# Kernel tuning notes

Hardware: AMD Instinct MI355X
Metric: run time of the kernel (lower is better)

## Reference

```python
import jax, jax.numpy as jnp
import numpy as np

D_HEAD = 64      # per-head dim (init d_head)
WINDOW = 64      # sliding_window_size
ROPE_BASE = 10000.0


def _rope(x):
    # x: [B, H, L, d] ; standard half-split rotary embedding over positions 0..L-1
    L, d = x.shape[-2], x.shape[-1]
    half = d // 2
    inv_freq = 1.0 / (ROPE_BASE ** (jnp.arange(half, dtype=jnp.float32) / half))
    ang = jnp.arange(L, dtype=jnp.float32)[:, None] * inv_freq  # [L, half]
    cos, sin = jnp.cos(ang), jnp.sin(ang)
    x1, x2 = x[..., :half], x[..., half:]
    return jnp.concatenate([x1 * cos - x2 * sin, x1 * sin + x2 * cos], axis=-1)


def setup_inputs() -> dict:
    key = jax.random.key(0)
    ks = jax.random.split(key, 4)
    B, L, D, H = 4, 2048, 2048, 2048
    nh = H // D_HEAD
    S = 16  # num_sinks
    u = jax.random.normal(ks[0], (B, L, D), jnp.float32)
    Wqkv = jax.random.normal(ks[1], (3 * H, D), jnp.float32) / np.sqrt(D)
    bqkv = jnp.zeros((3 * H,), jnp.float32)
    Wo = jax.random.normal(ks[2], (D, H), jnp.float32) / np.sqrt(H)
    bo = jnp.zeros((D,), jnp.float32)
    sinks = jax.random.normal(ks[3], (nh, S, D_HEAD), jnp.float32) / np.sqrt(D_HEAD)
    return {"u": u, "Wqkv": Wqkv, "bqkv": bqkv, "Wo": Wo, "bo": bo, "sinks": sinks}


def reference(u, Wqkv, bqkv, Wo, bo, sinks):
    B, L, D = u.shape
    d, w = D_HEAD, WINDOW
    nh, S, _ = sinks.shape
    scale = 1.0 / np.sqrt(d)

    qkv = u @ Wqkv.T + bqkv                         # [B, L, 3H]
    q, k, v = jnp.split(qkv, 3, axis=-1)
    heads = lambda x: x.reshape(B, L, nh, d).transpose(0, 2, 1, 3)  # [B, nh, L, d]
    q, k, v = heads(q), heads(k), heads(v)
    q, k = _rope(q), _rope(k)

    # Banded (sliding-window) attention in blocks of size w: query block i
    # attends key blocks {i-1, i, i+1} plus S global sink tokens.
    # Sink queries (prepended in the original) are discarded by O[:, :, -L:],
    # so we only compute attention for the L real queries.
    nb = L // w
    Qb = q.reshape(B, nh, nb, w, d)
    Kb = k.reshape(B, nh, nb, w, d)
    Vb = v.reshape(B, nh, nb, w, d)

    blk = jnp.arange(nb)[:, None] + jnp.arange(-1, 2)[None, :]   # [nb, 3]
    valid = (blk >= 0) & (blk < nb)
    blkc = jnp.clip(blk, 0, nb - 1)
    Kband = Kb[:, :, blkc].reshape(B, nh, nb, 3 * w, d)
    Vband = Vb[:, :, blkc].reshape(B, nh, nb, 3 * w, d)

    qpos = (jnp.arange(nb) * w)[:, None] + jnp.arange(w)          # [nb, w]
    kpos = ((blkc * w)[..., None] + jnp.arange(w)).reshape(nb, 3 * w)
    vmask = jnp.broadcast_to(valid[:, :, None], (nb, 3, w)).reshape(nb, 3 * w)
    mask = vmask[:, None, :] & (jnp.abs(qpos[:, :, None] - kpos[:, None, :]) <= w)  # [nb, w, 3w]

    s_band = jnp.einsum('bhnqd,bhnkd->bhnqk', Qb, Kband) * scale
    s_band = jnp.where(mask, s_band, -jnp.inf)
    s_sink = jnp.einsum('bhnqd,hsd->bhnqs', Qb, sinks) * scale    # sink K = sink param (no RoPE)
    p = jax.nn.softmax(jnp.concatenate([s_sink, s_band], axis=-1), axis=-1)

    O = (jnp.einsum('bhnqs,hsd->bhnqd', p[..., :S], sinks)        # sink V = sink param
         + jnp.einsum('bhnqk,bhnkd->bhnqd', p[..., S:], Vband))
    y = O.reshape(B, nh, L, d).transpose(0, 2, 1, 3).reshape(B, L, nh * d)
    return y @ Wo.T + bo
```

## Files before the change

kernel.cpp:

```cpp
#include <hip/hip_runtime.h>
#include <hip/hip_bf16.h>

typedef unsigned short u16;
typedef __attribute__((ext_vector_type(8))) short bf16x8;
typedef __attribute__((ext_vector_type(4))) float f32x4;

__device__ __forceinline__ u16 f2b(float f) {
  union { __hip_bfloat16 h; u16 u; } cv;
  cv.h = __float2bfloat16(f);
  return cv.u;
}
__device__ __forceinline__ float b2f(u16 u) {
  union { unsigned int i; float f; } cv;
  cv.i = ((unsigned int)u) << 16;
  return cv.f;
}

__global__ void cvt_bf16(const float* __restrict__ in, u16* __restrict__ out) {
  size_t i = ((size_t)blockIdx.x * 256 + threadIdx.x) * 4;
  float4 v = *(const float4*)(in + i);
  ushort4 o;
  o.x = f2b(v.x); o.y = f2b(v.y); o.z = f2b(v.z); o.w = f2b(v.w);
  *(ushort4*)(out + i) = o;
}

__global__ void rope_tab_k(float2* __restrict__ tab) {
  int t = blockIdx.x * 256 + threadIdx.x;
  int l = t >> 5, i = t & 31;
  float inv = powf(10000.0f, -(float)i * (1.0f / 32.0f));
  float ang = (float)l * inv;
  tab[t] = make_float2(cosf(ang), sinf(ang));
}

template<int NCOLS, bool ROPE>
__global__ __launch_bounds__(512, 2) void gemm_p(const u16* __restrict__ A,
                                                 const u16* __restrict__ Bm,
                                                 const float* __restrict__ bias,
                                                 u16* __restrict__ Cb,
                                                 float* __restrict__ Cf,
                                                 const float2* __restrict__ tab) {
  extern __shared__ char smem[];
  u16* Asl = (u16*)smem;
  u16* Bsl = (u16*)(smem + 65536);
  const int tid = threadIdx.x, lane = tid & 63, w = tid >> 6;
  const int wr = w >> 2, wcn = w & 3;
  const int fr = lane & 15, fk = lane >> 4;
  const int m0 = blockIdx.y * 256, n0 = blockIdx.x * 256;
  const int srow = lane >> 2;
  const int gslot = (lane & 3) ^ ((lane >> 3) & 3);
  const int c0 = w * 2, c1 = c0 + 1;
  const int sel = (fr >> 1) & 3;
  const int ka = (fk ^ sel) << 4;
  f32x4 acc[8][4] = {};

  auto stage = [&](int jj) {
    int slot = jj & 3;
    int kk = jj * 32 + gslot * 8;
    u16* Ad = Asl + slot * 8192;
    u16* Bd = Bsl + slot * 8192;
    const u16* gA0 = A  + (size_t)(m0 + c0 * 16 + srow) * 2048 + kk;
    const u16* gA1 = A  + (size_t)(m0 + c1 * 16 + srow) * 2048 + kk;
    const u16* gB0 = Bm + (size_t)(n0 + c0 * 16 + srow) * 2048 + kk;
    const u16* gB1 = Bm + (size_t)(n0 + c1 * 16 + srow) * 2048 + kk;
    __builtin_amdgcn_global_load_lds((const __attribute__((address_space(1))) unsigned int*)gA0,
        (__attribute__((address_space(3))) unsigned int*)(Ad + c0 * 512), 16, 0, 0);
    __builtin_amdgcn_global_load_lds((const __attribute__((address_space(1))) unsigned int*)gA1,
        (__attribute__((address_space(3))) unsigned int*)(Ad + c1 * 512), 16, 0, 0);
    __builtin_amdgcn_global_load_lds((const __attribute__((address_space(1))) unsigned int*)gB0,
        (__attribute__((address_space(3))) unsigned int*)(Bd + c0 * 512), 16, 0, 0);
    __builtin_amdgcn_global_load_lds((const __attribute__((address_space(1))) unsigned int*)gB1,
        (__attribute__((address_space(3))) unsigned int*)(Bd + c1 * 512), 16, 0, 0);
  };

  stage(0); stage(1); stage(2);
  asm volatile("s_waitcnt vmcnt(8)" ::: "memory");
  asm volatile("s_barrier" ::: "memory");

  for (int j = 0; j < 64; ++j) {
    if (j < 61) stage(j + 3);
    const char* Ab = (const char*)(Asl + (j & 3) * 8192);
    const char* Bb = (const char*)(Bsl + (j & 3) * 8192);
    bf16x8 af[8], bv[4];
    #pragma unroll
    for (int n = 0; n < 4; ++n)
      bv[n] = *(const bf16x8*)(Bb + (wcn * 64 + n * 16 + fr) * 64 + ka);
    #pragma unroll
    for (int m = 0; m < 8; ++m)
      af[m] = *(const bf16x8*)(Ab + (wr * 128 + m * 16 + fr) * 64 + ka);
    asm volatile("s_barrier" ::: "memory");
    asm volatile("s_waitcnt lgkmcnt(0)" ::: "memory");
    __builtin_amdgcn_sched_barrier(0);
    __builtin_amdgcn_s_setprio(1);
    #pragma unroll
    for (int m = 0; m < 8; ++m)
      #pragma unroll
      for (int n = 0; n < 4; ++n)
        acc[m][n] = __builtin_amdgcn_mfma_f32_16x16x32_bf16(af[m], bv[n], acc[m][n], 0, 0, 0);
    __builtin_amdgcn_s_setprio(0);
    __builtin_amdgcn_sched_barrier(0);
    if (j < 61)       asm volatile("s_waitcnt vmcnt(8)" ::: "memory");
    else if (j == 61) asm volatile("s_waitcnt vmcnt(4)" ::: "memory");
    else if (j == 62) asm volatile("s_waitcnt vmcnt(0)" ::: "memory");
    asm volatile("s_barrier" ::: "memory");
  }

  #pragma unroll
  for (int m = 0; m < 8; ++m) {
    int grow0 = m0 + wr * 128 + m * 16 + fk * 4;
    #pragma unroll
    for (int n = 0; n < 4; ++n) {
      int gcol = n0 + wcn * 64 + n * 16 + fr;
      if (ROPE) {
        if (gcol < 4096) {
          int c = gcol & 63;
          int i = c & 31;
          bool lo = c < 32;
          float bx = bias[gcol], bp = bias[gcol ^ 32];
          #pragma unroll
          for (int r = 0; r < 4; ++r) {
            int t = grow0 + r;
            float2 cs = tab[((t & 2047) << 5) + i];
            float xb = acc[m][n][r] + bx;
            float pb = acc[m][n ^ 2][r] + bp;
            float o = lo ? (xb * cs.x - pb * cs.y) : (pb * cs.y + xb * cs.x);
            Cb[(size_t)t * NCOLS + gcol] = f2b(o);
          }
        } else {
          float bx = bias[gcol];
          #pragma unroll
          for (int r = 0; r < 4; ++r)
            Cb[(size_t)(grow0 + r) * NCOLS + gcol] = f2b(acc[m][n][r] + bx);
        }
      } else {
        float bx = bias[gcol];
        #pragma unroll
        for (int r = 0; r < 4; ++r)
          Cf[(size_t)(grow0 + r) * NCOLS + gcol] = acc[m][n][r] + bx;
      }
    }
  }
}

#define PSTR 232
__global__ __launch_bounds__(256) void attn_k(const u16* __restrict__ qkv,
                                              const float* __restrict__ sinks,
                                              u16* __restrict__ O) {
  extern __shared__ char smem[];
  char* Kraw = smem;
  char* Qraw = smem + 28672;
  u16* Ps = (u16*)smem;
  u16* Vt = (u16*)(smem + 29696);
  char* tmpb = smem + 62464;
  const int tid = threadIdx.x, lane = tid & 63, wid = tid >> 6;
  const int fr = lane & 15, fk = lane >> 4;
  const int bx = blockIdx.x;
  const int n = bx & 31, h = (bx >> 5) & 31, b = bx >> 10;
  const size_t qrow0 = (size_t)b * 2048 + n * 64;

  for (int c = tid; c < 512; c += 256) {
    int row = c >> 3, colb = (c & 7) * 16;
    uint4 v = *(const uint4*)((const char*)(qkv + (qrow0 + row) * 6144 + h * 64) + colb);
    *(uint4*)(Qraw + ((row * 128 + colb) ^ ((row & 7) << 4))) = v;
  }
  {
    int row = tid >> 4, col4 = (tid & 15) * 4;
    float4 v = *(const float4*)(sinks + ((size_t)h * 16 + row) * 64 + col4);
    ushort4 o; o.x = f2b(v.x); o.y = f2b(v.y); o.z = f2b(v.z); o.w = f2b(v.w);
    *(ushort4*)(Kraw + ((row * 128 + col4 * 2) ^ ((row & 7) << 4))) = o;
  }
  for (int c = tid; c < 1536; c += 256) {
    int kidx = c >> 3, colb = (c & 7) * 16;
    int blk = n - 1 + (kidx >> 6);
    int blkc = min(max(blk, 0), 31);
    int kpos = blkc * 64 + (kidx & 63);
    uint4 v = *(const uint4*)((const char*)(qkv + ((size_t)b * 2048 + kpos) * 6144 + 2048 + h * 64) + colb);
    int row = 16 + kidx;
    *(uint4*)(Kraw + ((row * 128 + colb) ^ ((row & 7) << 4))) = v;
  }
  if (tid < 128) {
    int row = 208 + (tid >> 3), colb = (tid & 7) * 16;
    uint4 z = {0, 0, 0, 0};
    *(uint4*)(Kraw + ((row * 128 + colb) ^ ((row & 7) << 4))) = z;
  }
  __syncthreads();

  bf16x8 qf[2];
  {
    int qrow = wid * 16 + fr;
    #pragma unroll
    for (int kc = 0; kc < 2; ++kc)
      qf[kc] = *(const bf16x8*)(Qraw + ((qrow * 128 + kc * 64 + fk * 16) ^ ((qrow & 7) << 4)));
  }
  f32x4 sacc[14];
  #pragma unroll
  for (int g = 0; g < 14; ++g) {
    int key = g * 16 + fr;
    bf16x8 kf0 = *(const bf16x8*)(Kraw + ((key * 128 + fk * 16) ^ ((key & 7) << 4)));
    bf16x8 kf1 = *(const bf16x8*)(Kraw + ((key * 128 + 64 + fk * 16) ^ ((key & 7) << 4)));
    f32x4 a = {};
    a = __builtin_amdgcn_mfma_f32_16x16x32_bf16(qf[0], kf0, a, 0, 0, 0);
    a = __builtin_amdgcn_mfma_f32_16x16x32_bf16(qf[1], kf1, a, 0, 0, 0);
    sacc[g] = a;
  }
  float rowmax[4] = {-3e38f, -3e38f, -3e38f, -3e38f};
  #pragma unroll
  for (int g = 0; g < 14; ++g) {
    int key = g * 16 + fr;
    #pragma unroll
    for (int r = 0; r < 4; ++r) {
      float s = sacc[g][r] * 0.125f;
      bool valid;
      if (key < 16) valid = true;
      else if (key < 208) {
        int kidx = key - 16;
        int blk = n - 1 + (kidx >> 6);
        int kpos = blk * 64 + (kidx & 63);
        int qpos = n * 64 + wid * 16 + fk * 4 + r;
        valid = (blk >= 0) && (blk < 32) && (qpos - kpos <= 64) && (kpos - qpos <= 64);
      } else valid = false;
      s = valid ? s : -1e30f;
      sacc[g][r] = s;
      rowmax[r] = fmaxf(rowmax[r], s);
    }
  }
  #pragma unroll
  for (int d = 1; d < 16; d <<= 1)
    #pragma unroll
    for (int r = 0; r < 4; ++r)
      rowmax[r] = fmaxf(rowmax[r], __shfl_xor(rowmax[r], d));
  float rowsum[4] = {0, 0, 0, 0};
  #pragma unroll
  for (int g = 0; g < 14; ++g)
    #pragma unroll
    for (int r = 0; r < 4; ++r) {
      float p = __expf(sacc[g][r] - rowmax[r]);
      sacc[g][r] = p;
      rowsum[r] += p;
    }
  #pragma unroll
  for (int d = 1; d < 16; d <<= 1)
    #pragma unroll
    for (int r = 0; r < 4; ++r)
      rowsum[r] += __shfl_xor(rowsum[r], d);
  __syncthreads();

  #pragma unroll
  for (int g = 0; g < 14; ++g)
    #pragma unroll
    for (int r = 0; r < 4; ++r)
      Ps[(wid * 16 + fk * 4 + r) * PSTR + g * 16 + fr] = f2b(sacc[g][r]);

  {
    u16* tw = (u16*)(tmpb + wid * 1088);
    const int g = lane >> 3, s = lane & 7;
    if (wid < 2) {
      int key = wid * 8 + g;
      float4 v0 = *(const float4*)(sinks + ((size_t)h * 16 + key) * 64 + s * 8);
      float4 v1 = *(const float4*)(sinks + ((size_t)h * 16 + key) * 64 + s * 8 + 4);
      u16* dst = tw + g * 68 + s * 8;
      dst[0] = f2b(v0.x); dst[1] = f2b(v0.y); dst[2] = f2b(v0.z); dst[3] = f2b(v0.w);
      dst[4] = f2b(v1.x); dst[5] = f2b(v1.y); dst[6] = f2b(v1.z); dst[7] = f2b(v1.w);
      u16 col[8];
      #pragma unroll
      for (int k = 0; k < 8; ++k) col[k] = tw[k * 68 + lane];
      *(bf16x8*)(Vt + lane * 256 + ((wid ^ (lane & 7)) * 8)) = *(bf16x8*)col;
    } else {
      bf16x8 z = {};
      *(bf16x8*)(Vt + lane * 256 + (((24 + wid) ^ (lane & 7)) * 8)) = z;
    }
    for (int it = 0; it < 6; ++it) {
      int kidx = it * 32 + wid * 8 + g;
      int blk = n - 1 + (kidx >> 6);
      int blkc = min(max(blk, 0), 31);
      int kpos = blkc * 64 + (kidx & 63);
      uint4 v = *(const uint4*)(qkv + ((size_t)b * 2048 + kpos) * 6144 + 4096 + h * 64 + s * 8);
      *(uint4*)(tw + g * 68 + s * 8) = v;
      u16 col[8];
      #pragma unroll
      for (int k = 0; k < 8; ++k) col[k] = tw[k * 68 + lane];
      int gi = 2 + it * 4 + wid;
      *(bf16x8*)(Vt + lane * 256 + ((gi ^ (lane & 7)) * 8)) = *(bf16x8*)col;
    }
  }
  __syncthreads();

  f32x4 oacc[4] = {};
  #pragma unroll
  for (int kc = 0; kc < 7; ++kc) {
    bf16x8 pf = *(const bf16x8*)(Ps + (wid * 16 + fr) * PSTR + kc * 32 + fk * 8);
    #pragma unroll
    for (int gd = 0; gd < 4; ++gd) {
      bf16x8 vf = *(const bf16x8*)(Vt + (gd * 16 + fr) * 256 + (((kc * 4 + fk) ^ (fr & 7)) * 8));
      oacc[gd] = __builtin_amdgcn_mfma_f32_16x16x32_bf16(pf, vf, oacc[gd], 0, 0, 0);
    }
  }
  #pragma unroll
  for (int gd = 0; gd < 4; ++gd)
    #pragma unroll
    for (int r = 0; r < 4; ++r) {
      int qrl = wid * 16 + fk * 4 + r;
      float v = oacc[gd][r] / rowsum[r];
      O[(qrow0 + qrl) * 2048 + h * 64 + gd * 16 + fr] = f2b(v);
    }
}

extern "C" void kernel_launch(void* const* d_in, const int* in_sizes, int n_in,
                              void* d_out, int out_size, void* d_ws, size_t ws_size,
                              hipStream_t stream) {
  const float* u     = (const float*)d_in[0];
  const float* Wqkv  = (const float*)d_in[1];
  const float* bqkv  = (const float*)d_in[2];
  const float* Wo    = (const float*)d_in[3];
  const float* bo    = (const float*)d_in[4];
  const float* sinks = (const float*)d_in[5];
  float* out = (float*)d_out;

  char* ws = (char*)d_ws;
  u16* u_bf   = (u16*)ws;
  u16* w1_bf  = (u16*)(ws + 33554432);
  u16* qkv_bf = (u16*)(ws + 58720256);
  float2* tab = (float2*)(ws + 159383552);
  u16* O_bf  = u_bf;
  u16* w2_bf = w1_bf;

  hipFuncSetAttribute((const void*)gemm_p<6144, true>,
                      hipFuncAttributeMaxDynamicSharedMemorySize, 131072);
  hipFuncSetAttribute((const void*)gemm_p<2048, false>,
                      hipFuncAttributeMaxDynamicSharedMemorySize, 131072);
  hipFuncSetAttribute((const void*)attn_k,
                      hipFuncAttributeMaxDynamicSharedMemorySize, 66816);

  cvt_bf16<<<16384, 256, 0, stream>>>(u, u_bf);
  cvt_bf16<<<12288, 256, 0, stream>>>(Wqkv, w1_bf);
  rope_tab_k<<<256, 256, 0, stream>>>(tab);
  gemm_p<6144, true><<<dim3(24, 32), 512, 131072, stream>>>(u_bf, w1_bf, bqkv, qkv_bf, nullptr, tab);
  attn_k<<<4096, 256, 66816, stream>>>(qkv_bf, sinks, O_bf);
  cvt_bf16<<<4096, 256, 0, stream>>>(Wo, w2_bf);
  gemm_p<2048, false><<<dim3(8, 32), 512, 131072, stream>>>(O_bf, w2_bf, bo, nullptr, out, nullptr);
}
```

Before: 521.3 us.

## Double-buffer GEMM register fragments to overlap LDS reads with MFMA

Unrolls the bf16 GEMM main loop by two and keeps two sets of A/B register fragments. LDS reads for step j+1 are issued while the MFMAs of step j run, and global-to-LDS staging now runs four steps ahead instead of three. Per-row global base pointers are hoisted out of the staging lambda. The aim is to hide LDS read latency and cut barrier stalls between k-steps, at the cost of higher VGPR pressure and more intricate waitcnt and barrier bookkeeping.

Measured after the change: 527.2 us. Within noise of the previous version (+1.1%).

```diff
diff --git a/kernel.cpp b/kernel.cpp
--- a/kernel.cpp
+++ b/kernel.cpp
@@ -52,57 +52,83 @@
   const int sel = (fr >> 1) & 3;
   const int ka = (fk ^ sel) << 4;
   f32x4 acc[8][4] = {};
+  bf16x8 afA[8], bvA[4], afB[8], bvB[4];
+
+  const u16* gA0 = A  + (size_t)(m0 + c0 * 16 + srow) * 2048 + gslot * 8;
+  const u16* gA1 = A  + (size_t)(m0 + c1 * 16 + srow) * 2048 + gslot * 8;
+  const u16* gB0 = Bm + (size_t)(n0 + c0 * 16 + srow) * 2048 + gslot * 8;
+  const u16* gB1 = Bm + (size_t)(n0 + c1 * 16 + srow) * 2048 + gslot * 8;
 
   auto stage = [&](int jj) {
     int slot = jj & 3;
-    int kk = jj * 32 + gslot * 8;
+    int kk = jj * 32;
     u16* Ad = Asl + slot * 8192;
     u16* Bd = Bsl + slot * 8192;
-    const u16* gA0 = A  + (size_t)(m0 + c0 * 16 + srow) * 2048 + kk;
-    const u16* gA1 = A  + (size_t)(m0 + c1 * 16 + srow) * 2048 + kk;
-    const u16* gB0 = Bm + (size_t)(n0 + c0 * 16 + srow) * 2048 + kk;
-    const u16* gB1 = Bm + (size_t)(n0 + c1 * 16 + srow) * 2048 + kk;
-    __builtin_amdgcn_global_load_lds((const __attribute__((address_space(1))) unsigned int*)gA0,
+    __builtin_amdgcn_global_load_lds((const __attribute__((address_space(1))) unsigned int*)(gA0 + kk),
         (__attribute__((address_space(3))) unsigned int*)(Ad + c0 * 512), 16, 0, 0);
-    __builtin_amdgcn_global_load_lds((const __attribute__((address_space(1))) unsigned int*)gA1,
+    __builtin_amdgcn_global_load_lds((const __attribute__((address_space(1))) unsigned int*)(gA1 + kk),
         (__attribute__((address_space(3))) unsigned int*)(Ad + c1 * 512), 16, 0, 0);
-    __builtin_amdgcn_global_load_lds((const __attribute__((address_space(1))) unsigned int*)gB0,
+    __builtin_amdgcn_global_load_lds((const __attribute__((address_space(1))) unsigned int*)(gB0 + kk),
         (__attribute__((address_space(3))) unsigned int*)(Bd + c0 * 512), 16, 0, 0);
-    __builtin_amdgcn_global_load_lds((const __attribute__((address_space(1))) unsigned int*)gB1,
+    __builtin_amdgcn_global_load_lds((const __attribute__((address_space(1))) unsigned int*)(gB1 + kk),
         (__attribute__((address_space(3))) unsigned int*)(Bd + c1 * 512), 16, 0, 0);
   };
 
-  stage(0); stage(1); stage(2);
+#define GP_READ(JJ, AF, BV) do {                                              \
+    const char* Ab_ = (const char*)(Asl + ((JJ) & 3) * 8192);                 \
+    const char* Bb_ = (const char*)(Bsl + ((JJ) & 3) * 8192);                 \
+    _Pragma("unroll")                                                         \
+    for (int n_ = 0; n_ < 4; ++n_)                                            \
+      BV[n_] = *(const bf16x8*)(Bb_ + (wcn * 64 + n_ * 16 + fr) * 64 + ka);   \
+    _Pragma("unroll")                                                         \
+    for (int m_ = 0; m_ < 8; ++m_)                                            \
+      AF[m_] = *(const bf16x8*)(Ab_ + (wr * 128 + m_ * 16 + fr) * 64 + ka);   \
+  } while (0)
+
+#define GP_MFMA(AF, BV) do {                                                  \
+    __builtin_amdgcn_s_setprio(1);                                            \
+    _Pragma("unroll")                                                         \
+    for (int m_ = 0; m_ < 8; ++m_)                                            \
+      _Pragma("unroll")                                                       \
+      for (int n_ = 0; n_ < 4; ++n_)                                          \
+        acc[m_][n_] = __builtin_amdgcn_mfma_f32_16x16x32_bf16(AF[m_], BV[n_], acc[m_][n_], 0, 0, 0); \
+    __builtin_amdgcn_s_setprio(0);                                            \
+  } while (0)
+
+#define GP_VM(P) do {                                                         \
+    if ((P) <= 59)      asm volatile("s_waitcnt vmcnt(8)" ::: "memory");      \
+    else if ((P) == 60) asm volatile("s_waitcnt vmcnt(4)" ::: "memory");      \
+    else                asm volatile("s_waitcnt vmcnt(0)" ::: "memory");      \
+  } while (0)
+
+  stage(0); stage(1); stage(2); stage(3);
   asm volatile("s_waitcnt vmcnt(8)" ::: "memory");
   asm volatile("s_barrier" ::: "memory");
-
-  for (int j = 0; j < 64; ++j) {
-    if (j < 61) stage(j + 3);
-    const char* Ab = (const char*)(Asl + (j & 3) * 8192);
-    const char* Bb = (const char*)(Bsl + (j & 3) * 8192);
-    bf16x8 af[8], bv[4];
-    #pragma unroll
-    for (int n = 0; n < 4; ++n)
-      bv[n] = *(const bf16x8*)(Bb + (wcn * 64 + n * 16 + fr) * 64 + ka);
-    #pragma unroll
-    for (int m = 0; m < 8; ++m)
-      af[m] = *(const bf16x8*)(Ab + (wr * 128 + m * 16 + fr) * 64 + ka);
+  GP_READ(0, afA, bvA);
+  asm volatile("s_waitcnt lgkmcnt(0)" ::: "memory");
+  asm volatile("s_barrier" ::: "memory");
+
+  for (int j = 0; j < 64; j += 2) {
+    if (j + 4 < 64) stage(j + 4);
+    GP_READ(j + 1, afB, bvB);
+    __builtin_amdgcn_sched_barrier(0);
+    GP_MFMA(afA, bvA);
+    asm volatile("s_waitcnt lgkmcnt(0)" ::: "memory");
+    GP_VM(j);
     asm volatile("s_barrier" ::: "memory");
-    asm volatile("s_waitcnt lgkmcnt(0)" ::: "memory");
+    if (j + 5 < 64) stage(j + 5);
+    if (j + 2 < 64) GP_READ(j + 2, afA, bvA);
     __builtin_amdgcn_sched_barrier(0);
-    __builtin_amdgcn_s_setprio(1);
-    #pragma unroll
-    for (int m = 0; m < 8; ++m)
-      #pragma unroll
-      for (int n = 0; n < 4; ++n)
-        acc[m][n] = __builtin_amdgcn_mfma_f32_16x16x32_bf16(af[m], bv[n], acc[m][n], 0, 0, 0);
-    __builtin_amdgcn_s_setprio(0);
-    __builtin_amdgcn_sched_barrier(0);
-    if (j < 61)       asm volatile("s_waitcnt vmcnt(8)" ::: "memory");
-    else if (j == 61) asm volatile("s_waitcnt vmcnt(4)" ::: "memory");
-    else if (j == 62) asm volatile("s_waitcnt vmcnt(0)" ::: "memory");
-    asm volatile("s_barrier" ::: "memory");
-  }
+    GP_MFMA(afB, bvB);
+    if (j + 2 < 64) {
+      asm volatile("s_waitcnt lgkmcnt(0)" ::: "memory");
+      GP_VM(j + 1);
+      asm volatile("s_barrier" ::: "memory");
+    }
+  }
+#undef GP_READ
+#undef GP_MFMA
+#undef GP_VM
 
   #pragma unroll
   for (int m = 0; m < 8; ++m) {
```
